# Kernel optimization log

Measured on AMD Instinct MI355X. Metric: run time of the kernel, lower is better.

The kernel has to match this reference:

```python
import jax, jax.numpy as jnp
import numpy as np

N_NODES = 100000
N_EDGES = 3200000
IN_CH, HIDDEN, OUT_CH = 256, 16, 16


def setup_inputs() -> dict:
    key = jax.random.key(0)
    k1, k2, k3, k4, k5, k6 = jax.random.split(key, 6)
    x = jax.random.normal(k1, (N_NODES, IN_CH), dtype=jnp.float32)
    edge_index = jax.random.randint(k2, (2, N_EDGES), 0, N_NODES, dtype=jnp.int64)
    W1 = jax.random.normal(k3, (IN_CH, HIDDEN), dtype=jnp.float32) * (1.0 / np.sqrt(IN_CH))
    b1 = jax.random.normal(k4, (HIDDEN,), dtype=jnp.float32) * 0.01
    W2 = jax.random.normal(k5, (HIDDEN, OUT_CH), dtype=jnp.float32) * (1.0 / np.sqrt(HIDDEN))
    b2 = jax.random.normal(k6, (OUT_CH,), dtype=jnp.float32) * 0.01
    return {"x": x, "edge_index": edge_index, "W1": W1, "b1": b1, "W2": W2, "b2": b2}


def gcn_layer(x, edge_index, W, b):
    # Linear projection: [N, in] @ [in, out] + b
    h = x @ W + b
    source, target = edge_index[0], edge_index[1]
    n = x.shape[0]
    # degree of target nodes (in-degree), symmetric normalization (Kipf & Welling 2017)
    deg = jax.ops.segment_sum(jnp.ones_like(target, dtype=h.dtype), target, num_segments=n)
    deg_inv_sqrt = jnp.where(deg > 0, jax.lax.rsqrt(jnp.maximum(deg, 1.0)), 0.0)
    norm = deg_inv_sqrt[source] * deg_inv_sqrt[target]  # [E]
    # gather-scale-scatter: msg = norm * h[source], aggregated by add at target
    msgs = norm[:, None] * h[source]  # [E, out]
    return jax.ops.segment_sum(msgs, target, num_segments=n)


def reference(x, edge_index, W1, b1, W2, b2):
    h = jax.nn.sigmoid(gcn_layer(x, edge_index, W1, b1))
    return jax.nn.sigmoid(gcn_layer(h, edge_index, W2, b2))
```

## Files before the change

### kernel.cpp

```cpp
#include <hip/hip_runtime.h>
#include <hip/hip_bf16.h>

#define IN_CH 256
#define HID 16
#define BS 256
#define CAP 9216
#define CHUNK 4096
#define PBLK 512
#define EPT (CHUNK/PBLK)
#define SORT_CAP CAP

typedef __attribute__((ext_vector_type(8))) short bf16x8;
typedef __attribute__((ext_vector_type(8))) short short8;
typedef __attribute__((ext_vector_type(4))) float floatx4;

static __device__ __forceinline__ short f2bf(float f) {
    __hip_bfloat16 h = __float2bfloat16(f);
    return *reinterpret_cast<short*>(&h);
}

static __device__ __forceinline__ void acc8(float* a, uint4 v) {
    unsigned w;
    w = v.x;
    a[0] += __uint_as_float(w << 16);
    a[1] += __uint_as_float(w & 0xffff0000u);
    w = v.y;
    a[2] += __uint_as_float(w << 16);
    a[3] += __uint_as_float(w & 0xffff0000u);
    w = v.z;
    a[4] += __uint_as_float(w << 16);
    a[5] += __uint_as_float(w & 0xffff0000u);
    w = v.w;
    a[6] += __uint_as_float(w << 16);
    a[7] += __uint_as_float(w & 0xffff0000u);
}

__global__ __launch_bounds__(PBLK) void k_part(
        const int* __restrict__ src, const int* __restrict__ tgt,
        int* __restrict__ gcursor, unsigned int* __restrict__ csr, int E, int nbuk) {
    __shared__ int lcount[512];
    __shared__ int gspan[512];
    int t = threadIdx.x;
    int base = blockIdx.x * CHUNK;

    lcount[t] = 0;
    __syncthreads();

    int ebuk[EPT], eofs[EPT];
    unsigned epk[EPT];
#pragma unroll
    for (int k = 0; k < EPT; k++) {
        int e = base + t + k * PBLK;
        if (e < E) {
            int s  = __builtin_nontemporal_load(src + e);
            int tg = __builtin_nontemporal_load(tgt + e);
            ebuk[k] = tg >> 8;
            epk[k] = ((unsigned)s << 8) | (unsigned)(tg & 255);
            eofs[k] = atomicAdd(&lcount[ebuk[k]], 1);
        } else {
            ebuk[k] = -1;
        }
    }
    __syncthreads();
    if (t < nbuk) {
        int c = lcount[t];
        if (c > 0) gspan[t] = atomicAdd(&gcursor[t], c);
    }
    __syncthreads();
#pragma unroll
    for (int k = 0; k < EPT; k++) {
        if (ebuk[k] >= 0) {
            int pos = gspan[ebuk[k]] + eofs[k];
            if (pos < CAP)
                csr[(size_t)ebuk[k] * CAP + pos] = epk[k];
        }
    }
}

__global__ __launch_bounds__(512, 4) void k_sortgemm(
        const unsigned int* __restrict__ csr, const int* __restrict__ gcursor,
        const float* __restrict__ x, const float* __restrict__ W1,
        const float* __restrict__ b1,
        int* __restrict__ csr2, int* __restrict__ rowptr,
        int* __restrict__ deg, float* __restrict__ dis,
        short* __restrict__ h1, int N) {
    __shared__ int lcnt[256];
    __shared__ int lscan[256];
    __shared__ float sdis[256];
    __shared__ int ssrc[SORT_CAP];
    int t = threadIdx.x, b = blockIdx.x;
    int start = b * CAP;
    int cnt = min(gcursor[b], CAP);
    int end = start + cnt;

    if (t < 256) lcnt[t] = 0;
    __syncthreads();
    for (int p = start + t; p < end; p += 512) atomicAdd(&lcnt[csr[p] & 255], 1);
    __syncthreads();
    int d = 0;
    if (t < 256) { d = lcnt[t]; lscan[t] = d; }
    __syncthreads();
    for (int off = 1; off < 256; off <<= 1) {
        int a = 0;
        if (t < 256 && t >= off) a = lscan[t - off];
        __syncthreads();
        if (t < 256) lscan[t] += a;
        __syncthreads();
    }
    if (t < 256) {
        int excl = lscan[t] - d;
        int n = b * BS + t;
        float dv = (d > 0) ? rsqrtf((float)d) : 0.0f;
        sdis[t] = dv;
        if (n < N) {
            rowptr[n] = start + excl;
            deg[n] = d;
            dis[n] = dv;
        }
        lcnt[t] = excl;
    }
    __syncthreads();
    for (int p = start + t; p < end; p += 512) {
        unsigned pk = csr[p];
        int pos = atomicAdd(&lcnt[pk & 255], 1);
        ssrc[pos] = (int)(pk >> 8);
    }
    __syncthreads();
    for (int i = t; i < cnt; i += 512) csr2[start + i] = ssrc[i];

    {
        int lane = t & 63, wave = t >> 6;
        int mc = lane & 15, q = lane >> 4;
        bf16x8 bfrag[8];
#pragma unroll
        for (int kb = 0; kb < 8; kb++) {
#pragma unroll
            for (int j = 0; j < 8; j++)
                bfrag[kb][j] = f2bf(W1[(kb * 32 + q * 8 + j) * HID + mc]);
        }
        float bias = b1[mc];
#pragma unroll
        for (int r2 = 0; r2 < 2; r2++) {
            int nb = b * BS + (wave * 2 + r2) * 16;
            if (nb < N) {
                const float* xrow = x + (size_t)(nb + mc) * IN_CH;
                floatx4 acc = {0.f, 0.f, 0.f, 0.f};
#pragma unroll
                for (int kb = 0; kb < 8; kb++) {
                    const floatx4* p = (const floatx4*)(xrow + kb * 32 + q * 8);
                    floatx4 v0 = __builtin_nontemporal_load(p);
                    floatx4 v1 = __builtin_nontemporal_load(p + 1);
                    bf16x8 afrag;
#pragma unroll
                    for (int j = 0; j < 4; j++) {
                        afrag[j]     = f2bf(v0[j]);
                        afrag[j + 4] = f2bf(v1[j]);
                    }
                    acc = __builtin_amdgcn_mfma_f32_16x16x32_bf16(afrag, bfrag[kb], acc, 0, 0, 0);
                }
#pragma unroll
                for (int r = 0; r < 4; r++) {
                    int node = nb + q * 4 + r;
                    h1[(size_t)node * HID + mc] = f2bf((acc[r] + bias) * sdis[node - b * BS]);
                }
            }
        }
    }
}

__global__ __launch_bounds__(256) void k_agg_mid(
        const short* __restrict__ h1, const int* __restrict__ csr2,
        const int* __restrict__ rowptr, const int* __restrict__ deg,
        const float* __restrict__ dis,
        const float* __restrict__ W2, const float* __restrict__ b2,
        short* __restrict__ h2, int N) {
    __shared__ float w2s[256];
    __shared__ float b2s[16];
    __shared__ float sv[128][17];
    int t = threadIdx.x;
    w2s[t] = W2[t];
    if (t < 16) b2s[t] = b2[t];
    int nl = t >> 1;
    int cg = t & 1;
    int n = blockIdx.x * 128 + nl;

    float a[8] = {0.f, 0.f, 0.f, 0.f, 0.f, 0.f, 0.f, 0.f};
    float d = 0.f;
    if (n < N) {
        d = dis[n];
        int start = rowptr[n], cnt = deg[n];
        const short* hb = h1 + 8 * cg;
        int i = start, end4 = start + (cnt & ~3), end = start + cnt;
        if (i < end4) {
            int s0 = csr2[i], s1 = csr2[i + 1], s2 = csr2[i + 2], s3 = csr2[i + 3];
            for (;;) {
                uint4 v0 = *(const uint4*)(hb + 16 * (size_t)s0);
                uint4 v1 = *(const uint4*)(hb + 16 * (size_t)s1);
                uint4 v2 = *(const uint4*)(hb + 16 * (size_t)s2);
                uint4 v3 = *(const uint4*)(hb + 16 * (size_t)s3);
                i += 4;
                bool more = (i < end4);
                int n0, n1, n2, n3;
                if (more) { n0 = csr2[i]; n1 = csr2[i + 1]; n2 = csr2[i + 2]; n3 = csr2[i + 3]; }
                acc8(a, v0); acc8(a, v1); acc8(a, v2); acc8(a, v3);
                if (!more) break;
                s0 = n0; s1 = n1; s2 = n2; s3 = n3;
            }
        }
        for (; i < end; i++) {
            uint4 v = *(const uint4*)(hb + 16 * (size_t)csr2[i]);
            acc8(a, v);
        }
    }
#pragma unroll
    for (int j = 0; j < 8; j++)
        sv[nl][8 * cg + j] = 1.0f / (1.0f + __expf(-d * a[j]));
    __syncthreads();
    if (n < N) {
        float o[8];
#pragma unroll
        for (int j = 0; j < 8; j++) o[j] = b2s[8 * cg + j];
#pragma unroll
        for (int k = 0; k < 16; k++) {
            float s = sv[nl][k];
#pragma unroll
            for (int j = 0; j < 8; j++) o[j] += s * w2s[k * 16 + 8 * cg + j];
        }
        short8 pk;
#pragma unroll
        for (int j = 0; j < 8; j++) pk[j] = f2bf(o[j] * d);
        *(short8*)(h2 + 16 * (size_t)n + 8 * cg) = pk;
    }
}

__global__ __launch_bounds__(256) void k_agg_out(
        const short* __restrict__ h2, const int* __restrict__ csr2,
        const int* __restrict__ rowptr, const int* __restrict__ deg,
        const float* __restrict__ dis, float* __restrict__ out, int N) {
    int t = threadIdx.x;
    int nl = t >> 1;
    int cg = t & 1;
    int n = blockIdx.x * 128 + nl;
    if (n >= N) return;
    float d = dis[n];
    int start = rowptr[n], cnt = deg[n];
    float a[8] = {0.f, 0.f, 0.f, 0.f, 0.f, 0.f, 0.f, 0.f};
    const short* hb = h2 + 8 * cg;
    int i = start, end4 = start + (cnt & ~3), end = start + cnt;
    if (i < end4) {
        int s0 = csr2[i], s1 = csr2[i + 1], s2 = csr2[i + 2], s3 = csr2[i + 3];
        for (;;) {
            uint4 v0 = *(const uint4*)(hb + 16 * (size_t)s0);
            uint4 v1 = *(const uint4*)(hb + 16 * (size_t)s1);
            uint4 v2 = *(const uint4*)(hb + 16 * (size_t)s2);
            uint4 v3 = *(const uint4*)(hb + 16 * (size_t)s3);
            i += 4;
            bool more = (i < end4);
            int n0, n1, n2, n3;
            if (more) { n0 = csr2[i]; n1 = csr2[i + 1]; n2 = csr2[i + 2]; n3 = csr2[i + 3]; }
            acc8(a, v0); acc8(a, v1); acc8(a, v2); acc8(a, v3);
            if (!more) break;
            s0 = n0; s1 = n1; s2 = n2; s3 = n3;
        }
    }
    for (; i < end; i++) {
        uint4 v = *(const uint4*)(hb + 16 * (size_t)csr2[i]);
        acc8(a, v);
    }
    floatx4 o0, o1;
#pragma unroll
    for (int j = 0; j < 4; j++) {
        o0[j] = 1.0f / (1.0f + __expf(-d * a[j]));
        o1[j] = 1.0f / (1.0f + __expf(-d * a[j + 4]));
    }
    float* op = out + 16 * (size_t)n + 8 * cg;
    *(floatx4*)op = o0;
    *(floatx4*)(op + 4) = o1;
}

extern "C" void kernel_launch(void* const* d_in, const int* in_sizes, int n_in,
                              void* d_out, int out_size, void* d_ws, size_t ws_size,
                              hipStream_t stream) {
    const float* x  = (const float*)d_in[0];
    const int*   ei = (const int*)d_in[1];
    const float* W1 = (const float*)d_in[2];
    const float* b1 = (const float*)d_in[3];
    const float* W2 = (const float*)d_in[4];
    const float* b2 = (const float*)d_in[5];
    float* out = (float*)d_out;

    int N = in_sizes[0] / IN_CH;
    int E = in_sizes[1] / 2;
    const int* src = ei;
    const int* tgt = ei + E;

    int NBUK = (N + BS - 1) / BS;

    char* ws = (char*)d_ws;
    auto align256 = [](size_t v) { return (v + 255) & ~(size_t)255; };
    size_t off = 0;
    int*          gcursor = (int*)(ws + off);          off += align256(512 * sizeof(int));
    unsigned int* csr     = (unsigned int*)(ws + off); off += align256((size_t)NBUK * CAP * sizeof(unsigned int));
    int*          csr2    = (int*)(ws + off);          off += align256((size_t)NBUK * CAP * sizeof(int));
    int*          rowptr  = (int*)(ws + off);          off += align256((size_t)N * sizeof(int));
    int*          deg     = (int*)(ws + off);          off += align256((size_t)N * sizeof(int));
    float*        dis     = (float*)(ws + off);        off += align256((size_t)N * sizeof(float));
    short*        h1      = (short*)(ws + off);        off += align256((size_t)N * HID * sizeof(short));
    short*        h2      = (short*)(ws + off);        off += align256((size_t)N * HID * sizeof(short));

    int grid_part = (E + CHUNK - 1) / CHUNK;
    int grid_ag   = (N + 127) / 128;

    hipMemsetAsync(gcursor, 0, 512 * sizeof(int), stream);
    k_part    <<<grid_part, PBLK, 0, stream>>>(src, tgt, gcursor, csr, E, NBUK);
    k_sortgemm<<<NBUK, 512, 0, stream>>>(csr, gcursor, x, W1, b1,
                                         csr2, rowptr, deg, dis, h1, N);
    k_agg_mid <<<grid_ag, 256, 0, stream>>>(h1, csr2, rowptr, deg, dis, W2, b2, h2, N);
    k_agg_out <<<grid_ag, 256, 0, stream>>>(h2, csr2, rowptr, deg, dis, out, N);
}
```

Before: 285.6 us.

## Split each node's edge list across four lanes in aggregation kernels

Both aggregation kernels now assign eight threads per node instead of two: four lanes stride over the neighbor list in parallel for each 8-channel half, then combine partial sums with xor shuffles. Each thread then computes and stores two output channels. The aim is more memory-level parallelism per node and less per-thread serial latency on degree-32 gathers. In exchange there are four times as many threads, shuffle reduction overhead, smaller blocks, and narrower stores.

Measured after the change: 271.8 us. 4.8% less time.

```diff
diff --git a/kernel.cpp b/kernel.cpp
--- a/kernel.cpp
+++ b/kernel.cpp
@@ -11,7 +11,6 @@
 #define SORT_CAP CAP
 
 typedef __attribute__((ext_vector_type(8))) short bf16x8;
-typedef __attribute__((ext_vector_type(8))) short short8;
 typedef __attribute__((ext_vector_type(4))) float floatx4;
 
 static __device__ __forceinline__ short f2bf(float f) {
@@ -176,13 +175,15 @@
         short* __restrict__ h2, int N) {
     __shared__ float w2s[256];
     __shared__ float b2s[16];
-    __shared__ float sv[128][17];
+    __shared__ float sv[32][17];
     int t = threadIdx.x;
     w2s[t] = W2[t];
     if (t < 16) b2s[t] = b2[t];
-    int nl = t >> 1;
-    int cg = t & 1;
-    int n = blockIdx.x * 128 + nl;
+    int nl  = t >> 3;
+    int sub = t & 7;
+    int cg  = sub & 1;
+    int par = sub >> 1;
+    int n = blockIdx.x * 32 + nl;
 
     float a[8] = {0.f, 0.f, 0.f, 0.f, 0.f, 0.f, 0.f, 0.f};
     float d = 0.f;
@@ -190,46 +191,38 @@
         d = dis[n];
         int start = rowptr[n], cnt = deg[n];
         const short* hb = h1 + 8 * cg;
-        int i = start, end4 = start + (cnt & ~3), end = start + cnt;
-        if (i < end4) {
-            int s0 = csr2[i], s1 = csr2[i + 1], s2 = csr2[i + 2], s3 = csr2[i + 3];
-            for (;;) {
-                uint4 v0 = *(const uint4*)(hb + 16 * (size_t)s0);
-                uint4 v1 = *(const uint4*)(hb + 16 * (size_t)s1);
-                uint4 v2 = *(const uint4*)(hb + 16 * (size_t)s2);
-                uint4 v3 = *(const uint4*)(hb + 16 * (size_t)s3);
-                i += 4;
-                bool more = (i < end4);
-                int n0, n1, n2, n3;
-                if (more) { n0 = csr2[i]; n1 = csr2[i + 1]; n2 = csr2[i + 2]; n3 = csr2[i + 3]; }
-                acc8(a, v0); acc8(a, v1); acc8(a, v2); acc8(a, v3);
-                if (!more) break;
-                s0 = n0; s1 = n1; s2 = n2; s3 = n3;
-            }
-        }
-        for (; i < end; i++) {
+        int i = start + par, end = start + cnt;
+        for (; i + 4 < end; i += 8) {
+            int s0 = csr2[i], s1 = csr2[i + 4];
+            uint4 v0 = *(const uint4*)(hb + 16 * (size_t)s0);
+            uint4 v1 = *(const uint4*)(hb + 16 * (size_t)s1);
+            acc8(a, v0); acc8(a, v1);
+        }
+        if (i < end) {
             uint4 v = *(const uint4*)(hb + 16 * (size_t)csr2[i]);
             acc8(a, v);
         }
     }
 #pragma unroll
-    for (int j = 0; j < 8; j++)
-        sv[nl][8 * cg + j] = 1.0f / (1.0f + __expf(-d * a[j]));
+    for (int j = 0; j < 8; j++) {
+        a[j] += __shfl_xor(a[j], 2);
+        a[j] += __shfl_xor(a[j], 4);
+    }
+    sv[nl][8 * cg + 2 * par]     = 1.0f / (1.0f + __expf(-d * a[2 * par]));
+    sv[nl][8 * cg + 2 * par + 1] = 1.0f / (1.0f + __expf(-d * a[2 * par + 1]));
     __syncthreads();
     if (n < N) {
-        float o[8];
-#pragma unroll
-        for (int j = 0; j < 8; j++) o[j] = b2s[8 * cg + j];
+        int oc = sub * 2;
+        float o0 = b2s[oc], o1 = b2s[oc + 1];
 #pragma unroll
         for (int k = 0; k < 16; k++) {
             float s = sv[nl][k];
-#pragma unroll
-            for (int j = 0; j < 8; j++) o[j] += s * w2s[k * 16 + 8 * cg + j];
-        }
-        short8 pk;
-#pragma unroll
-        for (int j = 0; j < 8; j++) pk[j] = f2bf(o[j] * d);
-        *(short8*)(h2 + 16 * (size_t)n + 8 * cg) = pk;
+            o0 += s * w2s[k * 16 + oc];
+            o1 += s * w2s[k * 16 + oc + 1];
+        }
+        unsigned pk = ((unsigned)(unsigned short)f2bf(o1 * d) << 16)
+                    | (unsigned)(unsigned short)f2bf(o0 * d);
+        *(unsigned int*)(h2 + 16 * (size_t)n + oc) = pk;
     }
 }
 
@@ -238,44 +231,36 @@
         const int* __restrict__ rowptr, const int* __restrict__ deg,
         const float* __restrict__ dis, float* __restrict__ out, int N) {
     int t = threadIdx.x;
-    int nl = t >> 1;
-    int cg = t & 1;
-    int n = blockIdx.x * 128 + nl;
+    int nl  = t >> 3;
+    int sub = t & 7;
+    int cg  = sub & 1;
+    int par = sub >> 1;
+    int n = blockIdx.x * 32 + nl;
     if (n >= N) return;
     float d = dis[n];
     int start = rowptr[n], cnt = deg[n];
     float a[8] = {0.f, 0.f, 0.f, 0.f, 0.f, 0.f, 0.f, 0.f};
     const short* hb = h2 + 8 * cg;
-    int i = start, end4 = start + (cnt & ~3), end = start + cnt;
-    if (i < end4) {
-        int s0 = csr2[i], s1 = csr2[i + 1], s2 = csr2[i + 2], s3 = csr2[i + 3];
-        for (;;) {
-            uint4 v0 = *(const uint4*)(hb + 16 * (size_t)s0);
-            uint4 v1 = *(const uint4*)(hb + 16 * (size_t)s1);
-            uint4 v2 = *(const uint4*)(hb + 16 * (size_t)s2);
-            uint4 v3 = *(const uint4*)(hb + 16 * (size_t)s3);
-            i += 4;
-            bool more = (i < end4);
-            int n0, n1, n2, n3;
-            if (more) { n0 = csr2[i]; n1 = csr2[i + 1]; n2 = csr2[i + 2]; n3 = csr2[i + 3]; }
-            acc8(a, v0); acc8(a, v1); acc8(a, v2); acc8(a, v3);
-            if (!more) break;
-            s0 = n0; s1 = n1; s2 = n2; s3 = n3;
-        }
-    }
-    for (; i < end; i++) {
+    int i = start + par, end = start + cnt;
+    for (; i + 4 < end; i += 8) {
+        int s0 = csr2[i], s1 = csr2[i + 4];
+        uint4 v0 = *(const uint4*)(hb + 16 * (size_t)s0);
+        uint4 v1 = *(const uint4*)(hb + 16 * (size_t)s1);
+        acc8(a, v0); acc8(a, v1);
+    }
+    if (i < end) {
         uint4 v = *(const uint4*)(hb + 16 * (size_t)csr2[i]);
         acc8(a, v);
     }
-    floatx4 o0, o1;
-#pragma unroll
-    for (int j = 0; j < 4; j++) {
-        o0[j] = 1.0f / (1.0f + __expf(-d * a[j]));
-        o1[j] = 1.0f / (1.0f + __expf(-d * a[j + 4]));
-    }
-    float* op = out + 16 * (size_t)n + 8 * cg;
-    *(floatx4*)op = o0;
-    *(floatx4*)(op + 4) = o1;
+#pragma unroll
+    for (int j = 0; j < 8; j++) {
+        a[j] += __shfl_xor(a[j], 2);
+        a[j] += __shfl_xor(a[j], 4);
+    }
+    float2 o;
+    o.x = 1.0f / (1.0f + __expf(-d * a[2 * par]));
+    o.y = 1.0f / (1.0f + __expf(-d * a[2 * par + 1]));
+    *(float2*)(out + 16 * (size_t)n + 8 * cg + 2 * par) = o;
 }
 
 extern "C" void kernel_launch(void* const* d_in, const int* in_sizes, int n_in,
@@ -309,7 +294,7 @@
     short*        h2      = (short*)(ws + off);        off += align256((size_t)N * HID * sizeof(short));
 
     int grid_part = (E + CHUNK - 1) / CHUNK;
-    int grid_ag   = (N + 127) / 128;
+    int grid_ag   = (N + 31) / 32;
 
     hipMemsetAsync(gcursor, 0, 512 * sizeof(int), stream);
     k_part    <<<grid_part, PBLK, 0, stream>>>(src, tgt, gcursor, csr, E, NBUK);
```
